# Performance work log

Measured on AMD Instinct MI355X. Metric: run time of the kernel, lower is better.

The kernel has to match this reference:

```python
import jax, jax.numpy as jnp
import numpy as np

B, D, H, W = 4, 64, 64, 64
S = 64          # number of attention segments
N = 8192        # query pixels
K = 4           # n_refs
HID = 256
D9 = D * 9      # feat_unfold 3x3
IN_DIM = D9 + 2 + 2  # +rel_coord +rel_cell


def setup_inputs() -> dict:
    key = jax.random.key(0)
    ks = jax.random.split(key, 10)
    feat = jax.random.normal(ks[0], (B, D, H, W), jnp.float32)
    attn_sftmx = jax.nn.softmax(jax.random.normal(ks[1], (B, H * W, S), jnp.float32), axis=2)
    coord = jax.random.uniform(ks[2], (B, N, 2), jnp.float32) * 2.0 - 1.0  # [-1,1]
    cell = jnp.full((B, N, 2), 2.0 / 256.0, jnp.float32)  # HR cell size for 256x256 output
    def lin(k, fi, fo):
        return jax.random.normal(k, (fi, fo), jnp.float32) / np.sqrt(fi).astype(np.float32)
    w0 = lin(ks[3], IN_DIM, HID); b0 = jnp.zeros((HID,), jnp.float32)
    w1 = lin(ks[4], HID, HID);    b1 = jnp.zeros((HID,), jnp.float32)
    w2 = lin(ks[5], HID, HID);    b2 = jnp.zeros((HID,), jnp.float32)
    w3 = lin(ks[6], HID, HID);    b3 = jnp.zeros((HID,), jnp.float32)
    w4 = lin(ks[7], HID, 3);      b4 = jnp.zeros((3,), jnp.float32)
    return dict(feat=feat, attn_sftmx=attn_sftmx, coord=coord, cell=cell,
                w0=w0, b0=b0, w1=w1, b1=b1, w2=w2, b2=b2, w3=w3, b3=b3, w4=w4, b4=b4)


def _imnet(x, w0, b0, w1, b1, w2, b2, w3, b3, w4, b4):
    h = jax.nn.relu(x @ w0 + b0)
    h = jax.nn.relu(h @ w1 + b1)
    h = jax.nn.relu(h @ w2 + b2)
    h = jax.nn.relu(h @ w3 + b3)
    return h @ w4 + b4


def reference(feat, attn_sftmx, coord, cell, w0, b0, w1, b1, w2, b2, w3, b3, w4, b4):
    Bn, Dc, h, w = feat.shape
    Nq = coord.shape[1]
    hw = h * w
    # ---- feat_unfold: F.unfold(feat, 3, padding=1) -> (B, D*9, h, w), channel order c*9 + ki*3 + kj
    pad = jnp.pad(feat, ((0, 0), (0, 0), (1, 1), (1, 1)))
    patches = jnp.stack([pad[:, :, ki:ki + h, kj:kj + w]
                         for ki in range(3) for kj in range(3)], axis=2)  # (B,D,9,h,w)
    d9 = Dc * 9
    feat_rows = patches.reshape(Bn, d9, h, w).transpose(0, 2, 3, 1).reshape(Bn, hw, d9)  # (B,hw,D9)
    scale_hw = jnp.array([h, w], jnp.float32)
    rel_cell = cell * scale_hw  # (B,N,2)

    # ================= attention ensemble =================
    pc = (coord + 1.0) / 2.0 * scale_hw
    pc = jnp.clip(pc.astype(jnp.int32), 0, hw - 1)
    pc1d = pc[..., 0] * h + pc[..., 1]  # (B,N)
    segm_idx_whole = jnp.argmax(attn_sftmx, axis=2)  # (B,hw)
    segm_idx = jnp.take_along_axis(segm_idx_whole, pc1d, axis=1)  # (B,N)
    attn_t = attn_sftmx.transpose(0, 2, 1)  # (B,S,hw)
    prob_map = jnp.take_along_axis(attn_t, segm_idx[:, :, None], axis=1)  # (B,N,hw)
    ref_probs, ref_coords = jax.lax.top_k(prob_map, K)  # (B,N,K)
    # Faithful to original: ref_coords (values in [0,hw)) index the FLATTENED (B*hw, D9)
    # feature table, i.e. all batches gather batch-0 rows (source-code behavior).
    ref_feats = feat_rows.reshape(Bn * hw, d9)[ref_coords]  # (B,N,K,D9)
    rrc = ref_coords - pc1d[..., None]  # (B,N,K) int
    rel0 = jnp.floor_divide(rrc, h).astype(jnp.float32) / h
    rel1 = jnp.mod(rrc, h).astype(jnp.float32) / w
    rel = jnp.stack([rel0, rel1], axis=-1)  # (B,N,K,2)
    rc_b = jnp.broadcast_to(rel_cell[:, :, None, :], (Bn, Nq, K, 2))
    inp_attn = jnp.concatenate([ref_feats, rel, rc_b], axis=-1)  # (B,N,K,IN)
    pred_attn = _imnet(inp_attn.reshape(-1, inp_attn.shape[-1]),
                       w0, b0, w1, b1, w2, b2, w3, b3, w4, b4).reshape(Bn, Nq, K, -1)
    wprob = ref_probs / jnp.sum(ref_probs, axis=-1, keepdims=True)
    ret_attn = jnp.sum(pred_attn * wprob[..., None], axis=2)  # (B,N,3)

    # ================= local ensemble =================
    rx, ry = 1.0 / h, 1.0 / w  # 2/h/2, 2/w/2
    eps = 1e-6
    offs = jnp.array([[-1., -1.], [-1., 1.], [1., -1.], [1., 1.]], jnp.float32) \
           * jnp.array([rx, ry], jnp.float32) + eps  # (4,2)
    c = jnp.clip(coord[None] + offs[:, None, None, :], -1 + 1e-6, 1 - 1e-6)  # (4,B,N,2)
    # grid_sample nearest, align_corners=False (grid flipped -> c[...,0] is height)
    iy = jnp.clip(jnp.rint(((c[..., 0] + 1.0) * h - 1.0) / 2.0), 0, h - 1).astype(jnp.int32)
    ix = jnp.clip(jnp.rint(((c[..., 1] + 1.0) * w - 1.0) / 2.0), 0, w - 1).astype(jnp.int32)
    flat = iy * w + ix  # (4,B,N)
    bidx = jnp.arange(Bn)[None, :, None]
    q_feat = feat_rows[bidx, flat]  # (4,B,N,D9)
    qc0 = -1.0 + (2.0 * iy.astype(jnp.float32) + 1.0) / h  # make_coord centers
    qc1 = -1.0 + (2.0 * ix.astype(jnp.float32) + 1.0) / w
    rel_coord = jnp.stack([(coord[None, ..., 0] - qc0) * h,
                           (coord[None, ..., 1] - qc1) * w], axis=-1)  # (4,B,N,2)
    rc_l = jnp.broadcast_to(rel_cell[None], (4, Bn, Nq, 2))
    inp_loc = jnp.concatenate([q_feat, rel_coord, rc_l], axis=-1)  # (4,B,N,IN)
    pred_loc = _imnet(inp_loc.reshape(-1, inp_loc.shape[-1]),
                      w0, b0, w1, b1, w2, b2, w3, b3, w4, b4).reshape(4, Bn, Nq, -1)
    area = jnp.abs(rel_coord[..., 0] * rel_coord[..., 1]) + 1e-9  # (4,B,N)
    tot = jnp.sum(area, axis=0)
    wts = area[::-1] / tot[None]  # area swap 0<->3, 1<->2 == reverse
    ret_local = jnp.sum(pred_loc * wts[..., None], axis=0)  # (B,N,3)

    total = float(K + 4)
    return ret_attn * (K / total) + ret_local * (4.0 / total)
```

## Files before the change

kernel.cpp:

```cpp
#include <hip/hip_runtime.h>
#include <hip/hip_bf16.h>
#include <math.h>
#include <stdint.h>

#define B_ 4
#define D_ 64
#define H_ 64
#define W_ 64
#define S_ 64
#define N_ 8192
#define K_ 4
#define HID_ 256
#define HW_ 4096
#define NQ_ (B_*N_)
#define ROWS_ (NQ_*8)

typedef _Float16 h8   __attribute__((ext_vector_type(8)));
typedef _Float16 h4   __attribute__((ext_vector_type(4)));
typedef __fp16   pk2  __attribute__((ext_vector_type(2)));
typedef float    f32x4 __attribute__((ext_vector_type(4)));

__global__ void fused_prep_kernel(const float* __restrict__ feat,
                                  const float* __restrict__ attn,
                                  const float* __restrict__ w0,
                                  const float* __restrict__ w1,
                                  const float* __restrict__ w2,
                                  const float* __restrict__ w3,
                                  const float* __restrict__ w4,
                                  _Float16* __restrict__ featT,
                                  float* __restrict__ attnT,
                                  _Float16* __restrict__ w0F,
                                  _Float16* __restrict__ wF123,
                                  float* __restrict__ w4T,
                                  float* __restrict__ w0tail,
                                  int* __restrict__ segm)
{
  __shared__ float t[64][65];
  int blk = blockIdx.x;
  int tid = threadIdx.x;

  if (blk < 256) {
    int b = blk >> 6, y = blk & 63;
    for (int p = 0; p < 16; ++p) {
      int c = p * 4 + (tid >> 6), x = tid & 63;
      t[c][x] = feat[(((size_t)b * 64 + c) << 12) + (y << 6) + x];
    }
    __syncthreads();
    for (int p = 0; p < 16; ++p) {
      int x = p * 4 + (tid >> 6), c = tid & 63;
      featT[((((size_t)b * 64 + y) * 64 + x) << 6) + c] = (_Float16)t[c][x];
    }
    return;
  }
  blk -= 256;
  if (blk < 256) {
    int b = blk >> 6, j0 = (blk & 63) << 6;
    for (int idx = tid; idx < 4096; idx += 256) {
      int r = idx >> 6, c = idx & 63;
      t[r][c] = attn[((size_t)(b * 4096 + j0 + r)) * 64 + c];
    }
    __syncthreads();
    for (int idx = tid; idx < 4096; idx += 256) {
      int s = idx >> 6, r = idx & 63;
      attnT[((size_t)(b * 64 + s)) * 4096 + j0 + r] = t[r][s];
    }
    return;
  }
  blk -= 256;
  if (blk < 1351) {
    int i = blk * 256 + tid;
    if (i < 147456) {
      int g = i / 36864, rem = i - g * 36864;
      int ks = rem >> 11, rem2 = rem & 2047;
      int cb = rem2 >> 9, e = rem2 & 511;
      int lane = e >> 3, j = e & 7;
      int n = g * 64 + cb * 16 + (lane & 15);
      int k = ks * 32 + (lane >> 4) * 8 + j;
      int kk = k >> 6, cc = k & 63;
      w0F[i] = (_Float16)w0[(cc * 9 + kk) * 256 + n];
      return;
    }
    i -= 147456;
    if (i < 196608) {
      int l = i >> 16, rem = i & 65535;
      int g = rem >> 14, rem2 = rem & 16383;
      int ks = rem2 >> 11, rem3 = rem2 & 2047;
      int cb = rem3 >> 9, e = rem3 & 511;
      int lane = e >> 3, j = e & 7;
      int n = g * 64 + cb * 16 + (lane & 15);
      int k = ks * 32 + (lane >> 4) * 8 + j;
      const float* w = (l == 0) ? w1 : (l == 1) ? w2 : w3;
      wF123[i] = (_Float16)w[k * 256 + n];
      return;
    }
    i -= 196608;
    if (i < 768) { int j = i / 256, c = i - j * 256; w4T[i] = w4[c * 3 + j]; return; }
    i -= 768;
    if (i < 1024) { int j = i >> 8, n = i & 255; w0tail[i] = w0[(576 + j) * 256 + n]; }
    return;
  }
  blk -= 1351;
  {
    int p = blk * 256 + tid;
    if (p >= B_ * HW_) return;
    const float* a = attn + (size_t)p * S_;
    float best = a[0]; int bi = 0;
    for (int s = 1; s < S_; ++s) { float v = a[s]; if (v > best) { best = v; bi = s; } }
    segm[p] = bi;
  }
}

__global__ void topk_kernel(const float* __restrict__ attnT,
                            int* __restrict__ refc, float* __restrict__ wprob)
{
  int bid = blockIdx.x;
  int tid = threadIdx.x;
  __shared__ float sv[256]; __shared__ int si[256];
  __shared__ float cvs[4]; __shared__ int cis[4];

  const float* col = attnT + (size_t)bid * 4096;
  float tv[4] = { -INFINITY, -INFINITY, -INFINITY, -INFINITY };
  int   ti[4] = { 0x7fffffff, 0x7fffffff, 0x7fffffff, 0x7fffffff };
  for (int j = tid; j < HW_; j += 256) {
    float v = col[j];
    if (v > tv[3]) {
      tv[3] = v; ti[3] = j;
      #pragma unroll
      for (int x = 3; x > 0; --x) {
        if (tv[x] > tv[x-1] || (tv[x] == tv[x-1] && ti[x] < ti[x-1])) {
          float fv = tv[x]; tv[x] = tv[x-1]; tv[x-1] = fv;
          int   fi = ti[x]; ti[x] = ti[x-1]; ti[x-1] = fi;
        }
      }
    }
  }
  int ptr = 0;
  for (int r = 0; r < 4; ++r) {
    sv[tid] = (ptr < 4) ? tv[ptr] : -INFINITY;
    si[tid] = (ptr < 4) ? ti[ptr] : 0x7fffffff;
    __syncthreads();
    for (int o = 128; o; o >>= 1) {
      if (tid < o) {
        float v2 = sv[tid + o]; int i2 = si[tid + o];
        if (v2 > sv[tid] || (v2 == sv[tid] && i2 < si[tid])) { sv[tid] = v2; si[tid] = i2; }
      }
      __syncthreads();
    }
    if (tid == 0) { cvs[r] = sv[0]; cis[r] = si[0]; }
    __syncthreads();
    if (ptr < 4 && ti[ptr] == cis[r]) ptr++;
    __syncthreads();
  }
  if (tid == 0) {
    float ssum = cvs[0] + cvs[1] + cvs[2] + cvs[3];
    for (int k = 0; k < 4; ++k) { refc[bid*4 + k] = cis[k]; wprob[bid*4 + k] = cvs[k] / ssum; }
  }
}

__global__ void meta_kernel(const float* __restrict__ coord, const float* __restrict__ cell,
                            const int* __restrict__ segm, const int* __restrict__ refc,
                            const float* __restrict__ wprob,
                            int* __restrict__ msrc, float4* __restrict__ mt,
                            float* __restrict__ mwgt)
{
  int q = blockIdx.x * 256 + threadIdx.x;
  if (q >= NQ_) return;
  int b = q >> 13;
  float c0 = coord[2*q], c1 = coord[2*q + 1];
  float rc0 = cell[2*q] * 64.0f, rc1 = cell[2*q + 1] * 64.0f;

  float pf0 = (c0 + 1.0f) / 2.0f * 64.0f;
  float pf1 = (c1 + 1.0f) / 2.0f * 64.0f;
  int pc0 = (int)pf0, pc1 = (int)pf1;
  pc0 = min(max(pc0, 0), 4095); pc1 = min(max(pc1, 0), 4095);
  int pc1d = pc0 * 64 + pc1;
  int sg = segm[b * 4096 + min(pc1d, 4095)];
  int base = (b * 64 + sg) * 4;
  #pragma unroll
  for (int k = 0; k < 4; ++k) {
    int rc = refc[base + k];
    int rrc = rc - pc1d;
    float rel0 = (float)(rrc >> 6) * 0.015625f;
    float rel1 = (float)(rrc & 63) * 0.015625f;
    int r = q * 8 + k;
    msrc[r] = rc;
    mt[r] = make_float4(rel0, rel1, rc0, rc1);
    mwgt[r] = 0.5f * wprob[base + k];
  }

  const float sg0[4] = { -1.f, -1.f, 1.f, 1.f };
  const float sg1[4] = { -1.f,  1.f, -1.f, 1.f };
  float area[4], rr0[4], rr1[4]; int srcs[4];
  #pragma unroll
  for (int t = 0; t < 4; ++t) {
    float o0 = sg0[t] * 0.015625f + 1e-6f;
    float o1 = sg1[t] * 0.015625f + 1e-6f;
    float cc0 = fminf(fmaxf(c0 + o0, -1.0f + 1e-6f), 1.0f - 1e-6f);
    float cc1 = fminf(fmaxf(c1 + o1, -1.0f + 1e-6f), 1.0f - 1e-6f);
    float vy = ((cc0 + 1.0f) * 64.0f - 1.0f) / 2.0f;
    float vx = ((cc1 + 1.0f) * 64.0f - 1.0f) / 2.0f;
    float fy = fminf(fmaxf(rintf(vy), 0.0f), 63.0f);
    float fx = fminf(fmaxf(rintf(vx), 0.0f), 63.0f);
    int iy = (int)fy, ix = (int)fx;
    srcs[t] = b * 4096 + iy * 64 + ix;
    float qc0 = -1.0f + (2.0f * (float)iy + 1.0f) / 64.0f;
    float qc1 = -1.0f + (2.0f * (float)ix + 1.0f) / 64.0f;
    float r0 = (c0 - qc0) * 64.0f;
    float r1 = (c1 - qc1) * 64.0f;
    rr0[t] = r0; rr1[t] = r1;
    area[t] = fabsf(r0 * r1) + 1e-9f;
  }
  float tot = area[0] + area[1] + area[2] + area[3];
  #pragma unroll
  for (int t = 0; t < 4; ++t) {
    int r = q * 8 + 4 + t;
    msrc[r] = srcs[t];
    mt[r] = make_float4(rr0[t], rr1[t], rc0, rc1);
    mwgt[r] = 0.5f * area[3 - t] / tot;
  }
}

__launch_bounds__(256, 2)
__global__ void p0_kernel(const _Float16* __restrict__ featT,
                          const _Float16* __restrict__ w0F,
                          _Float16* __restrict__ P0h)
{
  int blk = blockIdx.x;
  int b = blk >> 7, y = (blk >> 1) & 63, hr = blk & 1;
  int tid = threadIdx.x;
  int wave = tid >> 6, lane = tid & 63, quad = lane >> 4, l16 = lane & 15;

  f32x4 acc[2][4];
  #pragma unroll
  for (int i = 0; i < 2; i++)
    #pragma unroll
    for (int j = 0; j < 4; j++) { f32x4 z = {0.f,0.f,0.f,0.f}; acc[i][j] = z; }
  h8 zero8 = {0,0,0,0,0,0,0,0};

  #pragma unroll
  for (int ks = 0; ks < 18; ++ks) {
    int k0 = ks * 32 + quad * 8;
    int kk = k0 >> 6, cc = k0 & 63;
    int di = kk / 3 - 1, dj = kk - (kk / 3) * 3 - 1;
    int yy = y + di;
    h8 afr[2];
    #pragma unroll
    for (int rb = 0; rb < 2; rb++) {
      int xx = hr * 32 + rb * 16 + l16 + dj;
      if ((unsigned)yy < 64u && (unsigned)xx < 64u)
        afr[rb] = *(const h8*)(featT + ((((size_t)b * 64 + yy) * 64 + xx) << 6) + cc);
      else
        afr[rb] = zero8;
    }
    h8 bfr[4];
    #pragma unroll
    for (int cb = 0; cb < 4; cb++)
      bfr[cb] = *(const h8*)(w0F + ((((size_t)wave * 18 + ks) * 4 + cb) << 9) + lane * 8);
    #pragma unroll
    for (int rb = 0; rb < 2; rb++)
      #pragma unroll
      for (int cb = 0; cb < 4; cb++)
        acc[rb][cb] = __builtin_amdgcn_mfma_f32_16x16x32_f16(afr[rb], bfr[cb], acc[rb][cb], 0, 0, 0);
  }
  int pixbase = b * 4096 + y * 64 + hr * 32;
  #pragma unroll
  for (int rb = 0; rb < 2; rb++)
    #pragma unroll
    for (int cb = 0; cb < 4; cb++)
      #pragma unroll
      for (int i = 0; i < 4; i++) {
        int m = rb * 16 + quad * 4 + i;
        int n = wave * 64 + cb * 16 + l16;
        P0h[((size_t)(pixbase + m) << 8) + n] = (_Float16)acc[rb][cb][i];
      }
}

__launch_bounds__(256, 2)
__global__ void trunk_kernel(const _Float16* __restrict__ P0h,
                             const int* __restrict__ msrc,
                             const float4* __restrict__ mt,
                             const float* __restrict__ mwgt,
                             const float* __restrict__ w0tail,
                             const float* __restrict__ b0,
                             const _Float16* __restrict__ wF123,
                             const float* __restrict__ b1,
                             const float* __restrict__ b2,
                             const float* __restrict__ b3,
                             const float* __restrict__ w4T,
                             const float* __restrict__ b4,
                             float* __restrict__ out)
{
  __shared__ _Float16 hS[128][264];
  __shared__ float mwL[128];
  __shared__ float swL[16];
  __shared__ float partB[16][3][4];

  int tid = threadIdx.x;
  int rowbase = blockIdx.x * 128;
  int wv = tid >> 6;

  if (tid < 128) mwL[tid] = mwgt[rowbase + tid];

  {
    int cg = tid & 63;
    float4 wt0 = ((const float4*)w0tail)[cg];
    float4 wt1 = ((const float4*)w0tail)[64 + cg];
    float4 wt2 = ((const float4*)w0tail)[128 + cg];
    float4 wt3 = ((const float4*)w0tail)[192 + cg];
    float4 bb  = ((const float4*)b0)[cg];
    #pragma unroll 1
    for (int g = 0; g < 4; ++g) {
      int srcs[8]; float4 ts[8];
      #pragma unroll
      for (int i = 0; i < 8; ++i) {
        int r = rowbase + g * 32 + i * 4 + wv;
        srcs[i] = msrc[r];
        ts[i] = mt[r];
      }
      #pragma unroll
      for (int i = 0; i < 8; ++i) {
        int rr = g * 32 + i * 4 + wv;
        float4 t = ts[i];
        h4 pvv = *(const h4*)(P0h + ((size_t)srcs[i] << 8) + cg * 4);
        float v0 = fmaxf((float)pvv[0] + t.x*wt0.x + t.y*wt1.x + t.z*wt2.x + t.w*wt3.x + bb.x, 0.0f);
        float v1 = fmaxf((float)pvv[1] + t.x*wt0.y + t.y*wt1.y + t.z*wt2.y + t.w*wt3.y + bb.y, 0.0f);
        float v2 = fmaxf((float)pvv[2] + t.x*wt0.z + t.y*wt1.z + t.z*wt2.z + t.w*wt3.z + bb.z, 0.0f);
        float v3 = fmaxf((float)pvv[3] + t.x*wt0.w + t.y*wt1.w + t.z*wt2.w + t.w*wt3.w + bb.w, 0.0f);
        pk2 a01 = __builtin_amdgcn_cvt_pkrtz(v0, v1);
        pk2 a23 = __builtin_amdgcn_cvt_pkrtz(v2, v3);
        int2 packed;
        packed.x = __builtin_bit_cast(int, a01);
        packed.y = __builtin_bit_cast(int, a23);
        *(int2*)(&hS[rr][cg * 4]) = packed;
      }
    }
  }
  __syncthreads();

  int wave = tid >> 6, lane = tid & 63, quad = lane >> 4, l16 = lane & 15;

  #pragma unroll 1
  for (int l = 0; l < 3; ++l) {
    const _Float16* wL = wF123 + (((size_t)l * 4 + wave) << 14);
    const float* bia = (l == 0) ? b1 : (l == 1) ? b2 : b3;
    float bv[4];
    #pragma unroll
    for (int cb = 0; cb < 4; cb++) bv[cb] = bia[wave * 64 + cb * 16 + l16];
    f32x4 acc[8][4];
    #pragma unroll
    for (int i = 0; i < 8; i++)
      #pragma unroll
      for (int j = 0; j < 4; j++) {
        f32x4 z = {bv[j], bv[j], bv[j], bv[j]};
        acc[i][j] = z;
      }

    h8 bP[2][4];
    #pragma unroll
    for (int cb = 0; cb < 4; cb++) {
      bP[0][cb] = *(const h8*)(wL + (((size_t)0 * 4 + cb) << 9) + lane * 8);
      bP[1][cb] = *(const h8*)(wL + (((size_t)1 * 4 + cb) << 9) + lane * 8);
    }

    #pragma unroll
    for (int ks = 0; ks < 8; ++ks) {
      int cur = ks & 1;
      int k0 = ks * 32 + quad * 8;
      h8 afr[8];
      #pragma unroll
      for (int rb = 0; rb < 8; rb++)
        afr[rb] = *(const h8*)(&hS[rb * 16 + l16][k0]);
      #pragma unroll
      for (int rb = 0; rb < 8; rb++)
        #pragma unroll
        for (int cb = 0; cb < 4; cb++)
          acc[rb][cb] = __builtin_amdgcn_mfma_f32_16x16x32_f16(afr[rb], bP[cur][cb], acc[rb][cb], 0, 0, 0);
      if (ks + 2 < 8) {
        #pragma unroll
        for (int cb = 0; cb < 4; cb++)
          bP[cur][cb] = *(const h8*)(wL + (((size_t)(ks + 2) * 4 + cb) << 9) + lane * 8);
      }
    }
    __syncthreads();
    #pragma unroll
    for (int rb = 0; rb < 8; rb++)
      #pragma unroll
      for (int cb = 0; cb < 4; cb++) {
        int n = wave * 64 + cb * 16 + l16;
        f32x4 a = acc[rb][cb];
        pk2 p01 = __builtin_amdgcn_cvt_pkrtz(fmaxf(a[0], 0.0f), fmaxf(a[1], 0.0f));
        pk2 p23 = __builtin_amdgcn_cvt_pkrtz(fmaxf(a[2], 0.0f), fmaxf(a[3], 0.0f));
        int m = rb * 16 + quad * 4;
        hS[m + 0][n] = (_Float16)p01[0];
        hS[m + 1][n] = (_Float16)p01[1];
        hS[m + 2][n] = (_Float16)p23[0];
        hS[m + 3][n] = (_Float16)p23[1];
      }
    __syncthreads();
  }

  {
    int q = tid >> 4, cpart = tid & 15;
    float accq[16];
    #pragma unroll
    for (int u = 0; u < 16; ++u) accq[u] = 0.0f;
    float sw = 0.0f;
    #pragma unroll
    for (int j = 0; j < 8; ++j) {
      int row = q * 8 + j;
      float w = mwL[row];
      sw += w;
      h8 a = *(const h8*)(&hS[row][cpart * 16]);
      h8 bq = *(const h8*)(&hS[row][cpart * 16 + 8]);
      #pragma unroll
      for (int u = 0; u < 8; ++u) {
        accq[u]     += w * (float)a[u];
        accq[8 + u] += w * (float)bq[u];
      }
    }
    __syncthreads();
    float* hsF = (float*)&hS[0][0];
    #pragma unroll
    for (int u = 0; u < 16; u += 4)
      *(f32x4*)(hsF + q * 256 + cpart * 16 + u) =
        f32x4{accq[u], accq[u+1], accq[u+2], accq[u+3]};
    if (cpart == 0) swL[q] = sw;
  }
  __syncthreads();
  if (tid < 192) {
    int q = tid / 12, r = tid % 12, j = r >> 2, part = r & 3;
    const float* hsF = (const float*)&hS[0][0];
    const float* hp = hsF + q * 256 + part * 64;
    const float* wp = w4T + j * 256 + part * 64;
    float s = 0.0f;
    #pragma unroll
    for (int u = 0; u < 64; ++u) s += hp[u] * wp[u];
    partB[q][j][part] = s;
  }
  __syncthreads();
  if (tid < 48) {
    int q = tid / 3, j = tid % 3;
    float o = partB[q][j][0] + partB[q][j][1] + partB[q][j][2] + partB[q][j][3]
            + b4[j] * swL[q];
    out[(size_t)(blockIdx.x * 16 + q) * 3 + j] = o;
  }
}

extern "C" void kernel_launch(void* const* d_in, const int* in_sizes, int n_in,
                              void* d_out, int out_size, void* d_ws, size_t ws_size,
                              hipStream_t stream)
{
  const float* feat  = (const float*)d_in[0];
  const float* attn  = (const float*)d_in[1];
  const float* coord = (const float*)d_in[2];
  const float* cell  = (const float*)d_in[3];
  const float* w0 = (const float*)d_in[4];
  const float* b0 = (const float*)d_in[5];
  const float* w1 = (const float*)d_in[6];
  const float* b1 = (const float*)d_in[7];
  const float* w2 = (const float*)d_in[8];
  const float* b2 = (const float*)d_in[9];
  const float* w3 = (const float*)d_in[10];
  const float* b3 = (const float*)d_in[11];
  const float* w4 = (const float*)d_in[12];
  const float* b4 = (const float*)d_in[13];
  float* out = (float*)d_out;

  char* ws = (char*)d_ws;
  size_t off = 0;
  auto alloc = [&](size_t bytes) -> char* {
    char* p = ws + off;
    off += (bytes + 255) & ~(size_t)255;
    return p;
  };
  _Float16* featT = (_Float16*)alloc((size_t)B_ * H_ * W_ * D_ * 2);
  _Float16* w0F   = (_Float16*)alloc((size_t)147456 * 2);
  _Float16* wF123 = (_Float16*)alloc((size_t)196608 * 2);
  float*  w4T   = (float*)alloc((size_t)3 * 256 * 4);
  float*  w0tl  = (float*)alloc((size_t)4 * 256 * 4);
  float*  attnT = (float*)alloc((size_t)B_ * S_ * HW_ * 4);
  int*    segm  = (int*)alloc((size_t)B_ * HW_ * 4);
  int*    refc  = (int*)alloc((size_t)B_ * S_ * K_ * 4);
  float*  wprob = (float*)alloc((size_t)B_ * S_ * K_ * 4);
  _Float16* P0h = (_Float16*)alloc((size_t)B_ * HW_ * 256 * 2);
  int*    msrc  = (int*)alloc((size_t)ROWS_ * 4);
  float4* mtb   = (float4*)alloc((size_t)ROWS_ * 16);
  float*  mwgt  = (float*)alloc((size_t)ROWS_ * 4);
  (void)in_sizes; (void)n_in; (void)out_size; (void)ws_size;

  fused_prep_kernel<<<1927, 256, 0, stream>>>(feat, attn, w0, w1, w2, w3, w4,
                                              featT, attnT, w0F, wF123, w4T, w0tl, segm);
  topk_kernel<<<256, 256, 0, stream>>>(attnT, refc, wprob);
  meta_kernel<<<128, 256, 0, stream>>>(coord, cell, segm, refc, wprob, msrc, mtb, mwgt);
  p0_kernel<<<512, 256, 0, stream>>>(featT, w0F, P0h);
  trunk_kernel<<<2048, 256, 0, stream>>>(P0h, msrc, mtb, mwgt, w0tl, b0, wF123,
                                         b1, b2, b3, w4T, b4, out);
}
```

Before: 270.4 us.

## Fuse per-query meta computation into trunk kernel and use wave-level top-k

Removes the separate meta kernel and its global msrc/mt/mwgt buffers by computing the per-query source indices, relative coordinates and weights inside the trunk kernel, staging them in shared memory. Rewrites top-k to use one wavefront per segment column, packing value and inverted index into 64-bit keys and merging with shuffles instead of shared-memory tree reductions over 256 threads. This saves one launch plus global round trips, at the cost of an extra barrier and serial 16-thread preamble per trunk block.

```diff
diff --git a/kernel.cpp b/kernel.cpp
--- a/kernel.cpp
+++ b/kernel.cpp
@@ -110,113 +110,54 @@
   }
 }
 
+__device__ inline void topk_insert(unsigned long long key,
+                                   unsigned long long& k0, unsigned long long& k1,
+                                   unsigned long long& k2, unsigned long long& k3)
+{
+  if (key > k3) {
+    if (key > k0)      { k3 = k2; k2 = k1; k1 = k0; k0 = key; }
+    else if (key > k1) { k3 = k2; k2 = k1; k1 = key; }
+    else if (key > k2) { k3 = k2; k2 = key; }
+    else               { k3 = key; }
+  }
+}
+
 __global__ void topk_kernel(const float* __restrict__ attnT,
                             int* __restrict__ refc, float* __restrict__ wprob)
 {
-  int bid = blockIdx.x;
-  int tid = threadIdx.x;
-  __shared__ float sv[256]; __shared__ int si[256];
-  __shared__ float cvs[4]; __shared__ int cis[4];
-
+  int wv = threadIdx.x >> 6, lane = threadIdx.x & 63;
+  int bid = blockIdx.x * 4 + wv;
   const float* col = attnT + (size_t)bid * 4096;
-  float tv[4] = { -INFINITY, -INFINITY, -INFINITY, -INFINITY };
-  int   ti[4] = { 0x7fffffff, 0x7fffffff, 0x7fffffff, 0x7fffffff };
-  for (int j = tid; j < HW_; j += 256) {
-    float v = col[j];
-    if (v > tv[3]) {
-      tv[3] = v; ti[3] = j;
-      #pragma unroll
-      for (int x = 3; x > 0; --x) {
-        if (tv[x] > tv[x-1] || (tv[x] == tv[x-1] && ti[x] < ti[x-1])) {
-          float fv = tv[x]; tv[x] = tv[x-1]; tv[x-1] = fv;
-          int   fi = ti[x]; ti[x] = ti[x-1]; ti[x-1] = fi;
-        }
-      }
-    }
-  }
-  int ptr = 0;
-  for (int r = 0; r < 4; ++r) {
-    sv[tid] = (ptr < 4) ? tv[ptr] : -INFINITY;
-    si[tid] = (ptr < 4) ? ti[ptr] : 0x7fffffff;
-    __syncthreads();
-    for (int o = 128; o; o >>= 1) {
-      if (tid < o) {
-        float v2 = sv[tid + o]; int i2 = si[tid + o];
-        if (v2 > sv[tid] || (v2 == sv[tid] && i2 < si[tid])) { sv[tid] = v2; si[tid] = i2; }
-      }
-      __syncthreads();
-    }
-    if (tid == 0) { cvs[r] = sv[0]; cis[r] = si[0]; }
-    __syncthreads();
-    if (ptr < 4 && ti[ptr] == cis[r]) ptr++;
-    __syncthreads();
-  }
-  if (tid == 0) {
-    float ssum = cvs[0] + cvs[1] + cvs[2] + cvs[3];
-    for (int k = 0; k < 4; ++k) { refc[bid*4 + k] = cis[k]; wprob[bid*4 + k] = cvs[k] / ssum; }
-  }
-}
-
-__global__ void meta_kernel(const float* __restrict__ coord, const float* __restrict__ cell,
-                            const int* __restrict__ segm, const int* __restrict__ refc,
-                            const float* __restrict__ wprob,
-                            int* __restrict__ msrc, float4* __restrict__ mt,
-                            float* __restrict__ mwgt)
-{
-  int q = blockIdx.x * 256 + threadIdx.x;
-  if (q >= NQ_) return;
-  int b = q >> 13;
-  float c0 = coord[2*q], c1 = coord[2*q + 1];
-  float rc0 = cell[2*q] * 64.0f, rc1 = cell[2*q + 1] * 64.0f;
-
-  float pf0 = (c0 + 1.0f) / 2.0f * 64.0f;
-  float pf1 = (c1 + 1.0f) / 2.0f * 64.0f;
-  int pc0 = (int)pf0, pc1 = (int)pf1;
-  pc0 = min(max(pc0, 0), 4095); pc1 = min(max(pc1, 0), 4095);
-  int pc1d = pc0 * 64 + pc1;
-  int sg = segm[b * 4096 + min(pc1d, 4095)];
-  int base = (b * 64 + sg) * 4;
+
+  unsigned long long k0 = 0, k1 = 0, k2 = 0, k3 = 0;
+  for (int it = 0; it < 64; ++it) {
+    int j = it * 64 + lane;
+    unsigned vb = __builtin_bit_cast(unsigned, col[j]);
+    unsigned long long key = ((unsigned long long)vb << 32) | (unsigned)(0xFFFFFFFFu - j);
+    topk_insert(key, k0, k1, k2, k3);
+  }
   #pragma unroll
-  for (int k = 0; k < 4; ++k) {
-    int rc = refc[base + k];
-    int rrc = rc - pc1d;
-    float rel0 = (float)(rrc >> 6) * 0.015625f;
-    float rel1 = (float)(rrc & 63) * 0.015625f;
-    int r = q * 8 + k;
-    msrc[r] = rc;
-    mt[r] = make_float4(rel0, rel1, rc0, rc1);
-    mwgt[r] = 0.5f * wprob[base + k];
-  }
-
-  const float sg0[4] = { -1.f, -1.f, 1.f, 1.f };
-  const float sg1[4] = { -1.f,  1.f, -1.f, 1.f };
-  float area[4], rr0[4], rr1[4]; int srcs[4];
-  #pragma unroll
-  for (int t = 0; t < 4; ++t) {
-    float o0 = sg0[t] * 0.015625f + 1e-6f;
-    float o1 = sg1[t] * 0.015625f + 1e-6f;
-    float cc0 = fminf(fmaxf(c0 + o0, -1.0f + 1e-6f), 1.0f - 1e-6f);
-    float cc1 = fminf(fmaxf(c1 + o1, -1.0f + 1e-6f), 1.0f - 1e-6f);
-    float vy = ((cc0 + 1.0f) * 64.0f - 1.0f) / 2.0f;
-    float vx = ((cc1 + 1.0f) * 64.0f - 1.0f) / 2.0f;
-    float fy = fminf(fmaxf(rintf(vy), 0.0f), 63.0f);
-    float fx = fminf(fmaxf(rintf(vx), 0.0f), 63.0f);
-    int iy = (int)fy, ix = (int)fx;
-    srcs[t] = b * 4096 + iy * 64 + ix;
-    float qc0 = -1.0f + (2.0f * (float)iy + 1.0f) / 64.0f;
-    float qc1 = -1.0f + (2.0f * (float)ix + 1.0f) / 64.0f;
-    float r0 = (c0 - qc0) * 64.0f;
-    float r1 = (c1 - qc1) * 64.0f;
-    rr0[t] = r0; rr1[t] = r1;
-    area[t] = fabsf(r0 * r1) + 1e-9f;
-  }
-  float tot = area[0] + area[1] + area[2] + area[3];
-  #pragma unroll
-  for (int t = 0; t < 4; ++t) {
-    int r = q * 8 + 4 + t;
-    msrc[r] = srcs[t];
-    mt[r] = make_float4(rr0[t], rr1[t], rc0, rc1);
-    mwgt[r] = 0.5f * area[3 - t] / tot;
+  for (int st = 1; st < 64; st <<= 1) {
+    unsigned long long p0 = __shfl_xor(k0, st, 64);
+    unsigned long long p1 = __shfl_xor(k1, st, 64);
+    unsigned long long p2 = __shfl_xor(k2, st, 64);
+    unsigned long long p3 = __shfl_xor(k3, st, 64);
+    topk_insert(p0, k0, k1, k2, k3);
+    topk_insert(p1, k0, k1, k2, k3);
+    topk_insert(p2, k0, k1, k2, k3);
+    topk_insert(p3, k0, k1, k2, k3);
+  }
+  if (lane == 0) {
+    unsigned long long ks[4] = { k0, k1, k2, k3 };
+    float vs[4]; int is[4];
+    #pragma unroll
+    for (int k = 0; k < 4; ++k) {
+      vs[k] = __builtin_bit_cast(float, (unsigned)(ks[k] >> 32));
+      is[k] = (int)(0xFFFFFFFFu - (unsigned)(ks[k] & 0xFFFFFFFFu));
+    }
+    float ssum = vs[0] + vs[1] + vs[2] + vs[3];
+    #pragma unroll
+    for (int k = 0; k < 4; ++k) { refc[bid*4 + k] = is[k]; wprob[bid*4 + k] = vs[k] / ssum; }
   }
 }
 
@@ -277,9 +218,11 @@
 
 __launch_bounds__(256, 2)
 __global__ void trunk_kernel(const _Float16* __restrict__ P0h,
-                             const int* __restrict__ msrc,
-                             const float4* __restrict__ mt,
-                             const float* __restrict__ mwgt,
+                             const float* __restrict__ coord,
+                             const float* __restrict__ cell,
+                             const int* __restrict__ segm,
+                             const int* __restrict__ refc,
+                             const float* __restrict__ wprob,
                              const float* __restrict__ w0tail,
                              const float* __restrict__ b0,
                              const _Float16* __restrict__ wF123,
@@ -291,15 +234,73 @@
                              float* __restrict__ out)
 {
   __shared__ _Float16 hS[128][264];
-  __shared__ float mwL[128];
-  __shared__ float swL[16];
-  __shared__ float partB[16][3][4];
+  __shared__ float  mwL[128];
+  __shared__ int    msrcL[128];
+  __shared__ float4 mtL[128];
+  __shared__ float  swL[16];
+  __shared__ float  partB[16][3][4];
 
   int tid = threadIdx.x;
   int rowbase = blockIdx.x * 128;
   int wv = tid >> 6;
 
-  if (tid < 128) mwL[tid] = mwgt[rowbase + tid];
+  if (tid < 16) {
+    int q = blockIdx.x * 16 + tid;
+    int b = q >> 13;
+    float c0 = coord[2*q], c1 = coord[2*q + 1];
+    float rc0 = cell[2*q] * 64.0f, rc1 = cell[2*q + 1] * 64.0f;
+
+    float pf0 = (c0 + 1.0f) / 2.0f * 64.0f;
+    float pf1 = (c1 + 1.0f) / 2.0f * 64.0f;
+    int pc0 = (int)pf0, pc1 = (int)pf1;
+    pc0 = min(max(pc0, 0), 4095); pc1 = min(max(pc1, 0), 4095);
+    int pc1d = pc0 * 64 + pc1;
+    int sg = segm[b * 4096 + min(pc1d, 4095)];
+    int base = (b * 64 + sg) * 4;
+    #pragma unroll
+    for (int k = 0; k < 4; ++k) {
+      int rc = refc[base + k];
+      int rrc = rc - pc1d;
+      float rel0 = (float)(rrc >> 6) * 0.015625f;
+      float rel1 = (float)(rrc & 63) * 0.015625f;
+      int rr = tid * 8 + k;
+      msrcL[rr] = rc;
+      mtL[rr] = make_float4(rel0, rel1, rc0, rc1);
+      mwL[rr] = 0.5f * wprob[base + k];
+    }
+
+    const float sg0[4] = { -1.f, -1.f, 1.f, 1.f };
+    const float sg1[4] = { -1.f,  1.f, -1.f, 1.f };
+    float area[4], rr0[4], rr1[4]; int srcs[4];
+    #pragma unroll
+    for (int t = 0; t < 4; ++t) {
+      float o0 = sg0[t] * 0.015625f + 1e-6f;
+      float o1 = sg1[t] * 0.015625f + 1e-6f;
+      float cc0 = fminf(fmaxf(c0 + o0, -1.0f + 1e-6f), 1.0f - 1e-6f);
+      float cc1 = fminf(fmaxf(c1 + o1, -1.0f + 1e-6f), 1.0f - 1e-6f);
+      float vy = ((cc0 + 1.0f) * 64.0f - 1.0f) / 2.0f;
+      float vx = ((cc1 + 1.0f) * 64.0f - 1.0f) / 2.0f;
+      float fy = fminf(fmaxf(rintf(vy), 0.0f), 63.0f);
+      float fx = fminf(fmaxf(rintf(vx), 0.0f), 63.0f);
+      int iy = (int)fy, ix = (int)fx;
+      srcs[t] = b * 4096 + iy * 64 + ix;
+      float qc0 = -1.0f + (2.0f * (float)iy + 1.0f) / 64.0f;
+      float qc1 = -1.0f + (2.0f * (float)ix + 1.0f) / 64.0f;
+      float r0 = (c0 - qc0) * 64.0f;
+      float r1 = (c1 - qc1) * 64.0f;
+      rr0[t] = r0; rr1[t] = r1;
+      area[t] = fabsf(r0 * r1) + 1e-9f;
+    }
+    float tot = area[0] + area[1] + area[2] + area[3];
+    #pragma unroll
+    for (int t = 0; t < 4; ++t) {
+      int rr = tid * 8 + 4 + t;
+      msrcL[rr] = srcs[t];
+      mtL[rr] = make_float4(rr0[t], rr1[t], rc0, rc1);
+      mwL[rr] = 0.5f * area[3 - t] / tot;
+    }
+  }
+  __syncthreads();
 
   {
     int cg = tid & 63;
@@ -313,9 +314,9 @@
       int srcs[8]; float4 ts[8];
       #pragma unroll
       for (int i = 0; i < 8; ++i) {
-        int r = rowbase + g * 32 + i * 4 + wv;
-        srcs[i] = msrc[r];
-        ts[i] = mt[r];
+        int rr_ = g * 32 + i * 4 + wv;
+        srcs[i] = msrcL[rr_];
+        ts[i] = mtL[rr_];
       }
       #pragma unroll
       for (int i = 0; i < 8; ++i) {
@@ -483,16 +484,12 @@
   int*    refc  = (int*)alloc((size_t)B_ * S_ * K_ * 4);
   float*  wprob = (float*)alloc((size_t)B_ * S_ * K_ * 4);
   _Float16* P0h = (_Float16*)alloc((size_t)B_ * HW_ * 256 * 2);
-  int*    msrc  = (int*)alloc((size_t)ROWS_ * 4);
-  float4* mtb   = (float4*)alloc((size_t)ROWS_ * 16);
-  float*  mwgt  = (float*)alloc((size_t)ROWS_ * 4);
   (void)in_sizes; (void)n_in; (void)out_size; (void)ws_size;
 
   fused_prep_kernel<<<1927, 256, 0, stream>>>(feat, attn, w0, w1, w2, w3, w4,
                                               featT, attnT, w0F, wF123, w4T, w0tl, segm);
-  topk_kernel<<<256, 256, 0, stream>>>(attnT, refc, wprob);
-  meta_kernel<<<128, 256, 0, stream>>>(coord, cell, segm, refc, wprob, msrc, mtb, mwgt);
+  topk_kernel<<<64, 256, 0, stream>>>(attnT, refc, wprob);
   p0_kernel<<<512, 256, 0, stream>>>(featT, w0F, P0h);
-  trunk_kernel<<<2048, 256, 0, stream>>>(P0h, msrc, mtb, mwgt, w0tl, b0, wF123,
-                                         b1, b2, b3, w4T, b4, out);
-}
+  trunk_kernel<<<2048, 256, 0, stream>>>(P0h, coord, cell, segm, refc, wprob,
+                                         w0tl, b0, wF123, b1, b2, b3, w4T, b4, out);
+}
```

Result: slower. 295.1 us (+9.1%).

## Fuse per-query metadata into trunk kernel and transpose MLP MFMA operands

Applied to the files above, without the earlier changes.

Removes the separate meta kernel and computes each query's eight row sources, relative coords and weights inside the trunk kernel's prologue, keeping them in shared memory instead of round-tripping through global buffers. Also swaps MFMA operand roles in the hidden layers so weights are the A operand and activations the B operand, which lets results be written back to LDS as packed 8-byte stores instead of scalar half stores. It saves one launch and global traffic, but adds a serialized 16-thread prologue plus a barrier at the start of every trunk block.

```diff
diff --git a/kernel.cpp b/kernel.cpp
--- a/kernel.cpp
+++ b/kernel.cpp
@@ -157,69 +157,6 @@
   }
 }
 
-__global__ void meta_kernel(const float* __restrict__ coord, const float* __restrict__ cell,
-                            const int* __restrict__ segm, const int* __restrict__ refc,
-                            const float* __restrict__ wprob,
-                            int* __restrict__ msrc, float4* __restrict__ mt,
-                            float* __restrict__ mwgt)
-{
-  int q = blockIdx.x * 256 + threadIdx.x;
-  if (q >= NQ_) return;
-  int b = q >> 13;
-  float c0 = coord[2*q], c1 = coord[2*q + 1];
-  float rc0 = cell[2*q] * 64.0f, rc1 = cell[2*q + 1] * 64.0f;
-
-  float pf0 = (c0 + 1.0f) / 2.0f * 64.0f;
-  float pf1 = (c1 + 1.0f) / 2.0f * 64.0f;
-  int pc0 = (int)pf0, pc1 = (int)pf1;
-  pc0 = min(max(pc0, 0), 4095); pc1 = min(max(pc1, 0), 4095);
-  int pc1d = pc0 * 64 + pc1;
-  int sg = segm[b * 4096 + min(pc1d, 4095)];
-  int base = (b * 64 + sg) * 4;
-  #pragma unroll
-  for (int k = 0; k < 4; ++k) {
-    int rc = refc[base + k];
-    int rrc = rc - pc1d;
-    float rel0 = (float)(rrc >> 6) * 0.015625f;
-    float rel1 = (float)(rrc & 63) * 0.015625f;
-    int r = q * 8 + k;
-    msrc[r] = rc;
-    mt[r] = make_float4(rel0, rel1, rc0, rc1);
-    mwgt[r] = 0.5f * wprob[base + k];
-  }
-
-  const float sg0[4] = { -1.f, -1.f, 1.f, 1.f };
-  const float sg1[4] = { -1.f,  1.f, -1.f, 1.f };
-  float area[4], rr0[4], rr1[4]; int srcs[4];
-  #pragma unroll
-  for (int t = 0; t < 4; ++t) {
-    float o0 = sg0[t] * 0.015625f + 1e-6f;
-    float o1 = sg1[t] * 0.015625f + 1e-6f;
-    float cc0 = fminf(fmaxf(c0 + o0, -1.0f + 1e-6f), 1.0f - 1e-6f);
-    float cc1 = fminf(fmaxf(c1 + o1, -1.0f + 1e-6f), 1.0f - 1e-6f);
-    float vy = ((cc0 + 1.0f) * 64.0f - 1.0f) / 2.0f;
-    float vx = ((cc1 + 1.0f) * 64.0f - 1.0f) / 2.0f;
-    float fy = fminf(fmaxf(rintf(vy), 0.0f), 63.0f);
-    float fx = fminf(fmaxf(rintf(vx), 0.0f), 63.0f);
-    int iy = (int)fy, ix = (int)fx;
-    srcs[t] = b * 4096 + iy * 64 + ix;
-    float qc0 = -1.0f + (2.0f * (float)iy + 1.0f) / 64.0f;
-    float qc1 = -1.0f + (2.0f * (float)ix + 1.0f) / 64.0f;
-    float r0 = (c0 - qc0) * 64.0f;
-    float r1 = (c1 - qc1) * 64.0f;
-    rr0[t] = r0; rr1[t] = r1;
-    area[t] = fabsf(r0 * r1) + 1e-9f;
-  }
-  float tot = area[0] + area[1] + area[2] + area[3];
-  #pragma unroll
-  for (int t = 0; t < 4; ++t) {
-    int r = q * 8 + 4 + t;
-    msrc[r] = srcs[t];
-    mt[r] = make_float4(rr0[t], rr1[t], rc0, rc1);
-    mwgt[r] = 0.5f * area[3 - t] / tot;
-  }
-}
-
 __launch_bounds__(256, 2)
 __global__ void p0_kernel(const _Float16* __restrict__ featT,
                           const _Float16* __restrict__ w0F,
@@ -277,9 +214,11 @@
 
 __launch_bounds__(256, 2)
 __global__ void trunk_kernel(const _Float16* __restrict__ P0h,
-                             const int* __restrict__ msrc,
-                             const float4* __restrict__ mt,
-                             const float* __restrict__ mwgt,
+                             const float* __restrict__ coord,
+                             const float* __restrict__ cell,
+                             const int* __restrict__ segm,
+                             const int* __restrict__ refc,
+                             const float* __restrict__ wprob,
                              const float* __restrict__ w0tail,
                              const float* __restrict__ b0,
                              const _Float16* __restrict__ wF123,
@@ -291,15 +230,72 @@
                              float* __restrict__ out)
 {
   __shared__ _Float16 hS[128][264];
-  __shared__ float mwL[128];
-  __shared__ float swL[16];
-  __shared__ float partB[16][3][4];
+  __shared__ float  mwL[128];
+  __shared__ int    msrcL[128];
+  __shared__ float4 mtL[128];
+  __shared__ float  swL[16];
+  __shared__ float  partB[16][3][4];
 
   int tid = threadIdx.x;
-  int rowbase = blockIdx.x * 128;
   int wv = tid >> 6;
 
-  if (tid < 128) mwL[tid] = mwgt[rowbase + tid];
+  if (tid < 16) {
+    int q = blockIdx.x * 16 + tid;
+    int b = q >> 13;
+    float c0 = coord[2*q], c1 = coord[2*q + 1];
+    float rc0 = cell[2*q] * 64.0f, rc1 = cell[2*q + 1] * 64.0f;
+
+    float pf0 = (c0 + 1.0f) / 2.0f * 64.0f;
+    float pf1 = (c1 + 1.0f) / 2.0f * 64.0f;
+    int pc0 = (int)pf0, pc1 = (int)pf1;
+    pc0 = min(max(pc0, 0), 4095); pc1 = min(max(pc1, 0), 4095);
+    int pc1d = pc0 * 64 + pc1;
+    int sg = segm[b * 4096 + min(pc1d, 4095)];
+    int base = (b * 64 + sg) * 4;
+    #pragma unroll
+    for (int k = 0; k < 4; ++k) {
+      int rc = refc[base + k];
+      int rrc = rc - pc1d;
+      float rel0 = (float)(rrc >> 6) * 0.015625f;
+      float rel1 = (float)(rrc & 63) * 0.015625f;
+      int rr = tid * 8 + k;
+      msrcL[rr] = rc;
+      mtL[rr] = make_float4(rel0, rel1, rc0, rc1);
+      mwL[rr] = 0.5f * wprob[base + k];
+    }
+
+    const float sg0[4] = { -1.f, -1.f, 1.f, 1.f };
+    const float sg1[4] = { -1.f,  1.f, -1.f, 1.f };
+    float area[4], rr0[4], rr1[4]; int srcs[4];
+    #pragma unroll
+    for (int t = 0; t < 4; ++t) {
+      float o0 = sg0[t] * 0.015625f + 1e-6f;
+      float o1 = sg1[t] * 0.015625f + 1e-6f;
+      float cc0 = fminf(fmaxf(c0 + o0, -1.0f + 1e-6f), 1.0f - 1e-6f);
+      float cc1 = fminf(fmaxf(c1 + o1, -1.0f + 1e-6f), 1.0f - 1e-6f);
+      float vy = ((cc0 + 1.0f) * 64.0f - 1.0f) / 2.0f;
+      float vx = ((cc1 + 1.0f) * 64.0f - 1.0f) / 2.0f;
+      float fy = fminf(fmaxf(rintf(vy), 0.0f), 63.0f);
+      float fx = fminf(fmaxf(rintf(vx), 0.0f), 63.0f);
+      int iy = (int)fy, ix = (int)fx;
+      srcs[t] = b * 4096 + iy * 64 + ix;
+      float qc0 = -1.0f + (2.0f * (float)iy + 1.0f) / 64.0f;
+      float qc1 = -1.0f + (2.0f * (float)ix + 1.0f) / 64.0f;
+      float r0 = (c0 - qc0) * 64.0f;
+      float r1 = (c1 - qc1) * 64.0f;
+      rr0[t] = r0; rr1[t] = r1;
+      area[t] = fabsf(r0 * r1) + 1e-9f;
+    }
+    float tot = area[0] + area[1] + area[2] + area[3];
+    #pragma unroll
+    for (int t = 0; t < 4; ++t) {
+      int rr = tid * 8 + 4 + t;
+      msrcL[rr] = srcs[t];
+      mtL[rr] = make_float4(rr0[t], rr1[t], rc0, rc1);
+      mwL[rr] = 0.5f * area[3 - t] / tot;
+    }
+  }
+  __syncthreads();
 
   {
     int cg = tid & 63;
@@ -313,9 +309,9 @@
       int srcs[8]; float4 ts[8];
       #pragma unroll
       for (int i = 0; i < 8; ++i) {
-        int r = rowbase + g * 32 + i * 4 + wv;
-        srcs[i] = msrc[r];
-        ts[i] = mt[r];
+        int rr_ = g * 32 + i * 4 + wv;
+        srcs[i] = msrcL[rr_];
+        ts[i] = mtL[rr_];
       }
       #pragma unroll
       for (int i = 0; i < 8; ++i) {
@@ -343,58 +339,57 @@
   for (int l = 0; l < 3; ++l) {
     const _Float16* wL = wF123 + (((size_t)l * 4 + wave) << 14);
     const float* bia = (l == 0) ? b1 : (l == 1) ? b2 : b3;
-    float bv[4];
-    #pragma unroll
-    for (int cb = 0; cb < 4; cb++) bv[cb] = bia[wave * 64 + cb * 16 + l16];
-    f32x4 acc[8][4];
-    #pragma unroll
-    for (int i = 0; i < 8; i++)
-      #pragma unroll
-      for (int j = 0; j < 4; j++) {
-        f32x4 z = {bv[j], bv[j], bv[j], bv[j]};
-        acc[i][j] = z;
-      }
-
-    h8 bP[2][4];
-    #pragma unroll
-    for (int cb = 0; cb < 4; cb++) {
-      bP[0][cb] = *(const h8*)(wL + (((size_t)0 * 4 + cb) << 9) + lane * 8);
-      bP[1][cb] = *(const h8*)(wL + (((size_t)1 * 4 + cb) << 9) + lane * 8);
+    f32x4 bvv[4];
+    #pragma unroll
+    for (int mb = 0; mb < 4; mb++)
+      bvv[mb] = *(const f32x4*)(bia + wave * 64 + mb * 16 + quad * 4);
+    f32x4 acc[4][8];
+    #pragma unroll
+    for (int mb = 0; mb < 4; mb++)
+      #pragma unroll
+      for (int nb = 0; nb < 8; nb++)
+        acc[mb][nb] = bvv[mb];
+
+    h8 wP[2][4];
+    #pragma unroll
+    for (int mb = 0; mb < 4; mb++) {
+      wP[0][mb] = *(const h8*)(wL + (((size_t)0 * 4 + mb) << 9) + lane * 8);
+      wP[1][mb] = *(const h8*)(wL + (((size_t)1 * 4 + mb) << 9) + lane * 8);
     }
 
     #pragma unroll
     for (int ks = 0; ks < 8; ++ks) {
       int cur = ks & 1;
       int k0 = ks * 32 + quad * 8;
-      h8 afr[8];
-      #pragma unroll
-      for (int rb = 0; rb < 8; rb++)
-        afr[rb] = *(const h8*)(&hS[rb * 16 + l16][k0]);
-      #pragma unroll
-      for (int rb = 0; rb < 8; rb++)
+      h8 hfr[8];
+      #pragma unroll
+      for (int nb = 0; nb < 8; nb++)
+        hfr[nb] = *(const h8*)(&hS[nb * 16 + l16][k0]);
+      #pragma unroll
+      for (int mb = 0; mb < 4; mb++)
         #pragma unroll
-        for (int cb = 0; cb < 4; cb++)
-          acc[rb][cb] = __builtin_amdgcn_mfma_f32_16x16x32_f16(afr[rb], bP[cur][cb], acc[rb][cb], 0, 0, 0);
+        for (int nb = 0; nb < 8; nb++)
+          acc[mb][nb] = __builtin_amdgcn_mfma_f32_16x16x32_f16(wP[cur][mb], hfr[nb], acc[mb][nb], 0, 0, 0);
       if (ks + 2 < 8) {
         #pragma unroll
-        for (int cb = 0; cb < 4; cb++)
-          bP[cur][cb] = *(const h8*)(wL + (((size_t)(ks + 2) * 4 + cb) << 9) + lane * 8);
-      }
-    }
-    __syncthreads();
-    #pragma unroll
-    for (int rb = 0; rb < 8; rb++)
-      #pragma unroll
-      for (int cb = 0; cb < 4; cb++) {
-        int n = wave * 64 + cb * 16 + l16;
-        f32x4 a = acc[rb][cb];
+        for (int mb = 0; mb < 4; mb++)
+          wP[cur][mb] = *(const h8*)(wL + (((size_t)(ks + 2) * 4 + mb) << 9) + lane * 8);
+      }
+    }
+    __syncthreads();
+    #pragma unroll
+    for (int mb = 0; mb < 4; mb++)
+      #pragma unroll
+      for (int nb = 0; nb < 8; nb++) {
+        f32x4 a = acc[mb][nb];
         pk2 p01 = __builtin_amdgcn_cvt_pkrtz(fmaxf(a[0], 0.0f), fmaxf(a[1], 0.0f));
         pk2 p23 = __builtin_amdgcn_cvt_pkrtz(fmaxf(a[2], 0.0f), fmaxf(a[3], 0.0f));
-        int m = rb * 16 + quad * 4;
-        hS[m + 0][n] = (_Float16)p01[0];
-        hS[m + 1][n] = (_Float16)p01[1];
-        hS[m + 2][n] = (_Float16)p23[0];
-        hS[m + 3][n] = (_Float16)p23[1];
+        int2 packed;
+        packed.x = __builtin_bit_cast(int, p01);
+        packed.y = __builtin_bit_cast(int, p23);
+        int row = nb * 16 + l16;
+        int ncol = wave * 64 + mb * 16 + quad * 4;
+        *(int2*)(&hS[row][ncol]) = packed;
       }
     __syncthreads();
   }
@@ -483,16 +478,12 @@
   int*    refc  = (int*)alloc((size_t)B_ * S_ * K_ * 4);
   float*  wprob = (float*)alloc((size_t)B_ * S_ * K_ * 4);
   _Float16* P0h = (_Float16*)alloc((size_t)B_ * HW_ * 256 * 2);
-  int*    msrc  = (int*)alloc((size_t)ROWS_ * 4);
-  float4* mtb   = (float4*)alloc((size_t)ROWS_ * 16);
-  float*  mwgt  = (float*)alloc((size_t)ROWS_ * 4);
   (void)in_sizes; (void)n_in; (void)out_size; (void)ws_size;
 
   fused_prep_kernel<<<1927, 256, 0, stream>>>(feat, attn, w0, w1, w2, w3, w4,
                                               featT, attnT, w0F, wF123, w4T, w0tl, segm);
   topk_kernel<<<256, 256, 0, stream>>>(attnT, refc, wprob);
-  meta_kernel<<<128, 256, 0, stream>>>(coord, cell, segm, refc, wprob, msrc, mtb, mwgt);
   p0_kernel<<<512, 256, 0, stream>>>(featT, w0F, P0h);
-  trunk_kernel<<<2048, 256, 0, stream>>>(P0h, msrc, mtb, mwgt, w0tl, b0, wF123,
-                                         b1, b2, b3, w4T, b4, out);
+  trunk_kernel<<<2048, 256, 0, stream>>>(P0h, coord, cell, segm, refc, wprob,
+                                         w0tl, b0, wF123, b1, b2, b3, w4T, b4, out);
 }
```

Result: faster. 244.5 us (-9.6%).
